# Performance work log

Measured on AMD Instinct MI355X. Metric: run time of the kernel, lower is better.

Reference implementation:

```python
import jax, jax.numpy as jnp
import numpy as np

B, N, M, C, H = 2, 256, 512, 256, 8
Dh = C // H          # head dim = 32
F = 256              # frequency_embedding_size
MAX_PERIOD = 10000.0


def setup_inputs() -> dict:
    rng = jax.random.key(0)
    ks = jax.random.split(rng, 12)
    s = 0.02

    def w(k, shape):
        return jax.random.normal(k, shape, jnp.float32) * s

    inp = {
        "query": jax.random.normal(ks[0], (B, N, C), jnp.float32),
        "key": jax.random.normal(ks[1], (B, M, C), jnp.float32),
        "query_pos": jax.random.uniform(ks[2], (B, N, M), jnp.float32),
        # attention projections (torch Linear stores W as (out,in))
        "Wq": w(ks[3], (C, C)), "bq": jnp.zeros((C,), jnp.float32),
        "Wk": w(ks[4], (C, C)),
        "Wv": w(ks[5], (C, C)), "bv": jnp.zeros((C,), jnp.float32),
        "Wo": w(ks[6], (C, C)), "bo": jnp.zeros((C,), jnp.float32),
        # ScalarEmbedder MLP: Linear(F, C) -> SiLU -> Linear(C, C)
        "W1": w(ks[7], (C, F)), "b1": jnp.zeros((C,), jnp.float32),
        "W2": w(ks[8], (C, C)), "b2": jnp.zeros((C,), jnp.float32),
        "freqs": jnp.exp(-np.log(MAX_PERIOD) * jnp.arange(F // 2, dtype=jnp.float32) / (F // 2)),
    }
    return inp


def reference(query, key, query_pos, Wq, bq, Wk, Wv, bv, Wo, bo, W1, b1, W2, b2, freqs):
    scale = Dh ** (-0.5)
    # projections -> (B, H, N/M, Dh)
    q = (query @ Wq.T + bq).reshape(B, N, H, Dh).transpose(0, 2, 1, 3)
    k = (key @ Wk.T).reshape(B, M, H, Dh).transpose(0, 2, 1, 3)
    v = (key @ Wv.T + bv).reshape(B, M, H, Dh).transpose(0, 2, 1, 3)
    # scalar positional embedding per (n, m) pair
    t = query_pos.reshape(-1)                              # (B*N*M,)
    tf = t[:, None] * freqs                                # (B*N*M, F/2)
    emb = jnp.concatenate([jnp.cos(tf), jnp.sin(tf)], -1)  # (B*N*M, F)
    pe = jax.nn.silu(emb @ W1.T + b1) @ W2.T + b2          # (B*N*M, C)
    pe = pe.reshape(B, N, M, H, Dh).transpose(0, 3, 1, 2, 4)  # (B,H,N,M,Dh)
    # gated scores: (q[:,:,:,None] * pe) . k  ==  einsum over d
    attn = jnp.einsum('bhnd,bhnmd,bhmd->bhnm', q, pe, k) * scale
    attn = jax.nn.softmax(attn, axis=-1)
    x = jnp.einsum('bhnm,bhmd->bhnd', attn, v)             # (B,H,N,Dh)
    x = x.transpose(0, 2, 1, 3).reshape(B, N, C)
    return x @ Wo.T + bo + query
```

## Files before the change

kernel.cpp:

```cpp
#include <hip/hip_runtime.h>

#define Bn 2
#define Nn 256
#define Mn 512
#define Cn 256
#define Hn 8
#define MT 64
#define SCALE_ 0.17677669529663687f

typedef short bf16x8 __attribute__((ext_vector_type(8)));
typedef float f32x4 __attribute__((ext_vector_type(4)));

static __device__ __forceinline__ float b2f(short s) {
    unsigned u = ((unsigned)(unsigned short)s) << 16;
    return __builtin_bit_cast(float, u);
}
static __device__ __forceinline__ short f2b(float f) {
    unsigned u = __builtin_bit_cast(unsigned, f);
    u += 0x7fffu + ((u >> 16) & 1u);
    return (short)(u >> 16);
}
static __device__ __forceinline__ void async16(const void* g, void* l) {
    __builtin_amdgcn_global_load_lds(
        (const __attribute__((address_space(1))) unsigned int*)g,
        (__attribute__((address_space(3))) unsigned int*)l, 16, 0, 0);
}

__global__ void convert_w(const float* __restrict__ W1, const float* __restrict__ W2,
                          short* __restrict__ W1b, short* __restrict__ W2b) {
    int i = blockIdx.x * 256 + threadIdx.x;
    W1b[i] = f2b(W1[i]);
    W2b[i] = f2b(W2[i]);
}

template <bool BF16OUT>
__global__ __launch_bounds__(256) void linear_rc(
        const float* __restrict__ A, const float* __restrict__ W,
        const float* __restrict__ bias, const float* __restrict__ res,
        float* __restrict__ outf, short* __restrict__ outb) {
    __shared__ float arow[32][Cn];
    const int r0 = blockIdx.x * 32;
    const int c0 = blockIdx.y * 64;
    const int t = threadIdx.x;
    #pragma unroll
    for (int i = 0; i < 32; ++i) arow[i][t] = A[(size_t)(r0 + i) * Cn + t];
    __syncthreads();
    const int col = c0 + (t & 63);
    const int rg = (t >> 6) * 8;
    float acc[8];
    #pragma unroll
    for (int i = 0; i < 8; ++i) acc[i] = 0.f;
    const float* wr = W + (size_t)col * Cn;
    for (int k = 0; k < Cn; k += 4) {
        const float4 wv = *(const float4*)(wr + k);
        #pragma unroll
        for (int i = 0; i < 8; ++i)
            acc[i] += arow[rg + i][k] * wv.x + arow[rg + i][k+1] * wv.y
                    + arow[rg + i][k+2] * wv.z + arow[rg + i][k+3] * wv.w;
    }
    const float bv = bias ? bias[col] : 0.f;
    #pragma unroll
    for (int i = 0; i < 8; ++i) {
        float o = acc[i] + bv;
        if (res) o += res[(size_t)(r0 + rg + i) * Cn + col];
        if (BF16OUT) outb[(size_t)(r0 + rg + i) * Cn + col] = f2b(o);
        else         outf[(size_t)(r0 + rg + i) * Cn + col] = o;
    }
}

__global__ __launch_bounds__(256) void linear_kv(
        const float* __restrict__ key, const float* __restrict__ Wk,
        const float* __restrict__ Wv, const float* __restrict__ bv,
        short* __restrict__ kpb, short* __restrict__ vpb) {
    __shared__ float arow[32][Cn];
    const int z = blockIdx.z;
    const float* W = z ? Wv : Wk;
    const float* bias = z ? bv : nullptr;
    short* outb = z ? vpb : kpb;
    const int r0 = blockIdx.x * 32;
    const int c0 = blockIdx.y * 64;
    const int t = threadIdx.x;
    #pragma unroll
    for (int i = 0; i < 32; ++i) arow[i][t] = key[(size_t)(r0 + i) * Cn + t];
    __syncthreads();
    const int col = c0 + (t & 63);
    const int rg = (t >> 6) * 8;
    float acc[8];
    #pragma unroll
    for (int i = 0; i < 8; ++i) acc[i] = 0.f;
    const float* wr = W + (size_t)col * Cn;
    for (int k = 0; k < Cn; k += 4) {
        const float4 wv = *(const float4*)(wr + k);
        #pragma unroll
        for (int i = 0; i < 8; ++i)
            acc[i] += arow[rg + i][k] * wv.x + arow[rg + i][k+1] * wv.y
                    + arow[rg + i][k+2] * wv.z + arow[rg + i][k+3] * wv.w;
    }
    const float bvv = bias ? bias[col] : 0.f;
    #pragma unroll
    for (int i = 0; i < 8; ++i)
        outb[(size_t)(r0 + rg + i) * Cn + col] = f2b(acc[i] + bvv);
}

__global__ __launch_bounds__(512, 1) void fused_attn(
        const float* __restrict__ qp, const short* __restrict__ kpb,
        const short* __restrict__ vpb, const float* __restrict__ qpos,
        const short* __restrict__ W1b, const short* __restrict__ W2b,
        const float* __restrict__ b1, const float* __restrict__ b2,
        const float* __restrict__ freqs, float* __restrict__ xout) {
    __shared__ __align__(16) char embS[MT * 512];
    __shared__ __align__(16) char kS[MT * 512];
    __shared__ __align__(16) char vS[MT * 512];
    __shared__ float tposS[Mn];
    __shared__ float scb2[Hn * MT];
    __shared__ float pacc[512];
    __shared__ float corrS[Hn], lS[Hn];

    const int t = threadIdx.x;
    const int lane = t & 63;
    const int w = t >> 6;
    const int lr = lane & 15, lg = lane >> 4;

    const int qrow = ((blockIdx.x & 7) << 6) | (blockIdx.x >> 3);
    const int b = qrow >> 8;

    bf16x8 w1r[16], w2r[16];
    #pragma unroll
    for (int jb = 0; jb < 2; ++jb) {
        const short* p1 = W1b + (size_t)(w * 32 + jb * 16 + lr) * Cn + lg * 8;
        const short* p2 = W2b + (size_t)(w * 32 + jb * 16 + lr) * Cn + lg * 8;
        #pragma unroll
        for (int kk = 0; kk < 8; ++kk) {
            w1r[jb * 8 + kk] = *(const bf16x8*)(p1 + kk * 32);
            w2r[jb * 8 + kk] = *(const bf16x8*)(p2 + kk * 32);
        }
    }
    const int cA = w * 32 + lr, cB = cA + 16;
    const float b1v0 = b1[cA], b1v1 = b1[cB];
    const float b2v0 = b2[cA], b2v1 = b2[cB];
    const float q0 = qp[(size_t)qrow * Cn + cA];
    const float q1 = qp[(size_t)qrow * Cn + cB];
    const float fv = freqs[t & 127];
    tposS[t] = qpos[(size_t)qrow * Mn + t];
    float m_run = -1e30f, l_run = 0.f;
    float xacc = 0.f;
    const f32x4 vzero = {0.f, 0.f, 0.f, 0.f};
    __syncthreads();

    for (int m0 = 0; m0 < Mn; m0 += MT) {
        {
            const size_t tbase = ((size_t)(b * Mn + m0)) * 512;
            #pragma unroll
            for (int i = 0; i < 4; ++i) {
                const int seg = (i * 8 + w) * 1024;
                async16((const char*)kpb + tbase + seg + lane * 16, kS + seg);
                async16((const char*)vpb + tbase + seg + lane * 16, vS + seg);
            }
        }

        {
            const int f = t & 127, mb = t >> 7;
            #pragma unroll 2
            for (int it = 0; it < 16; ++it) {
                const int m = it * 4 + mb;
                const float tv = tposS[m0 + m];
                float sv, cv;
                __sincosf(tv * fv, &sv, &cv);
                char* rowp = embS + m * 512;
                const int sw = (m & 7) << 4;
                *(short*)(rowp + ((f * 2) ^ sw)) = f2b(cv);
                *(short*)(rowp + ((256 + f * 2) ^ sw)) = f2b(sv);
            }
        }
        __syncthreads();

        f32x4 acc[4][2];
        #pragma unroll
        for (int pb = 0; pb < 4; ++pb) { acc[pb][0] = vzero; acc[pb][1] = vzero; }
        #pragma unroll
        for (int pb = 0; pb < 4; ++pb) {
            const int row = pb * 16 + lr;
            const int sw = (row & 7) << 4;
            const char* rowp = embS + row * 512;
            #pragma unroll
            for (int kk = 0; kk < 8; ++kk) {
                const bf16x8 a = *(const bf16x8*)(rowp + ((lg * 16 + kk * 64) ^ sw));
                acc[pb][0] = __builtin_amdgcn_mfma_f32_16x16x32_bf16(a, w1r[kk],     acc[pb][0], 0, 0, 0);
                acc[pb][1] = __builtin_amdgcn_mfma_f32_16x16x32_bf16(a, w1r[8 + kk], acc[pb][1], 0, 0, 0);
            }
        }
        __syncthreads();

        #pragma unroll
        for (int pb = 0; pb < 4; ++pb) {
            #pragma unroll
            for (int jb = 0; jb < 2; ++jb) {
                const float bv = jb ? b1v1 : b1v0;
                const int j = w * 32 + jb * 16 + lr;
                #pragma unroll
                for (int r = 0; r < 4; ++r) {
                    const int row = pb * 16 + lg * 4 + r;
                    float hv = acc[pb][jb][r] + bv;
                    hv = hv / (1.f + __expf(-hv));
                    *(short*)(embS + row * 512 + ((j * 2) ^ ((row & 7) << 4))) = f2b(hv);
                }
            }
        }
        __syncthreads();

        #pragma unroll
        for (int pb = 0; pb < 4; ++pb) { acc[pb][0] = vzero; acc[pb][1] = vzero; }
        #pragma unroll
        for (int pb = 0; pb < 4; ++pb) {
            const int row = pb * 16 + lr;
            const int sw = (row & 7) << 4;
            const char* rowp = embS + row * 512;
            #pragma unroll
            for (int kk = 0; kk < 8; ++kk) {
                const bf16x8 a = *(const bf16x8*)(rowp + ((lg * 16 + kk * 64) ^ sw));
                acc[pb][0] = __builtin_amdgcn_mfma_f32_16x16x32_bf16(a, w2r[kk],     acc[pb][0], 0, 0, 0);
                acc[pb][1] = __builtin_amdgcn_mfma_f32_16x16x32_bf16(a, w2r[8 + kk], acc[pb][1], 0, 0, 0);
            }
        }

        #pragma unroll
        for (int pb = 0; pb < 4; ++pb) {
            #pragma unroll
            for (int r = 0; r < 4; ++r) {
                const int m = pb * 16 + lg * 4 + r;
                const float k0 = b2f(*(const short*)(kS + m * 512 + cA * 2));
                const float k1 = b2f(*(const short*)(kS + m * 512 + cB * 2));
                float v = (acc[pb][0][r] + b2v0) * q0 * k0
                        + (acc[pb][1][r] + b2v1) * q1 * k1;
                v += __shfl_xor(v, 1);
                v += __shfl_xor(v, 2);
                v += __shfl_xor(v, 4);
                v += __shfl_xor(v, 8);
                if (lr == 0) scb2[w * MT + m] = v * SCALE_;
            }
        }

        {
            const float s = scb2[w * MT + lane];
            float tmax = s;
            #pragma unroll
            for (int msk = 1; msk < 64; msk <<= 1) tmax = fmaxf(tmax, __shfl_xor(tmax, msk));
            const float mnew = fmaxf(m_run, tmax);
            const float corr = __expf(m_run - mnew);
            const float e = __expf(s - mnew);
            scb2[w * MT + lane] = e;
            float ss = e;
            #pragma unroll
            for (int msk = 1; msk < 64; msk <<= 1) ss += __shfl_xor(ss, msk);
            l_run = l_run * corr + ss;
            m_run = mnew;
            if (lane == 0) corrS[w] = corr;
        }
        __syncthreads();

        {
            const int c = t & 255, half = t >> 8;
            const int h = c >> 5;
            const char* vb = vS + (half * 32) * 512 + c * 2;
            const float* wr2 = scb2 + h * MT + half * 32;
            float s = 0.f;
            #pragma unroll 8
            for (int m = 0; m < 32; ++m)
                s += wr2[m] * b2f(*(const short*)(vb + m * 512));
            pacc[t] = s;
        }
        __syncthreads();
        if (t < 256) xacc = xacc * corrS[t >> 5] + pacc[t] + pacc[t + 256];
        __syncthreads();
    }

    if (lane == 0) lS[w] = l_run;
    __syncthreads();
    if (t < 256) xout[(size_t)qrow * Cn + t] = xacc / lS[t >> 5];
}

extern "C" void kernel_launch(void* const* d_in, const int* in_sizes, int n_in,
                              void* d_out, int out_size, void* d_ws, size_t ws_size,
                              hipStream_t stream) {
    const float* query = (const float*)d_in[0];
    const float* key   = (const float*)d_in[1];
    const float* qpos  = (const float*)d_in[2];
    const float* Wq    = (const float*)d_in[3];
    const float* bq    = (const float*)d_in[4];
    const float* Wk    = (const float*)d_in[5];
    const float* Wv    = (const float*)d_in[6];
    const float* bv    = (const float*)d_in[7];
    const float* Wo    = (const float*)d_in[8];
    const float* bo    = (const float*)d_in[9];
    const float* W1    = (const float*)d_in[10];
    const float* b1    = (const float*)d_in[11];
    const float* W2    = (const float*)d_in[12];
    const float* b2    = (const float*)d_in[13];
    const float* freqs = (const float*)d_in[14];
    float* out = (float*)d_out;

    char* ws = (char*)d_ws;
    float* qp  = (float*)(ws);
    short* kpb = (short*)(ws + 524288);
    short* vpb = (short*)(ws + 1048576);
    float* xo  = (float*)(ws + 1572864);
    short* W1b = (short*)(ws + 2097152);
    short* W2b = (short*)(ws + 2228224);

    convert_w<<<256, 256, 0, stream>>>(W1, W2, W1b, W2b);
    linear_rc<false><<<dim3(16, 4), 256, 0, stream>>>(query, Wq, bq, nullptr, qp, nullptr);
    linear_kv<<<dim3(32, 4, 2), 256, 0, stream>>>(key, Wk, Wv, bv, kpb, vpb);
    fused_attn<<<Bn * Nn, 512, 0, stream>>>(qp, kpb, vpb, qpos, W1b, W2b, b1, b2, freqs, xo);
    linear_rc<false><<<dim3(16, 4), 256, 0, stream>>>(xo, Wo, bo, query, out, nullptr);
}
```

Before: 316.4 us.

## Merge prep kernels, transpose K/V layout, vectorize sincos and V reduction

Combines the weight conversion and the Q/K/V projection kernels into one prep launch, and writes K and V transposed (channel-major, bf16) so the attention kernel can do vector LDS reads through a swizzled padded layout. Each thread now computes 16 sincos values for one row and stores them as 16-byte vectors. It also sets waves_per_eu to 2 and pins the weight registers with empty asm. One barrier at the end of the m-loop is dropped. The intent is to cut launch overhead and the scalar LDS traffic in the embedding, score and PV stages. The cost is more registers per thread, and removing the barrier may create a race on pacc and scb2 between iterations.

New measurement: 299.8 us. 1.06x faster.

```diff
diff --git a/kernel.cpp b/kernel.cpp
--- a/kernel.cpp
+++ b/kernel.cpp
@@ -9,6 +9,7 @@
 #define SCALE_ 0.17677669529663687f
 
 typedef short bf16x8 __attribute__((ext_vector_type(8)));
+typedef short bf16x4 __attribute__((ext_vector_type(4)));
 typedef float f32x4 __attribute__((ext_vector_type(4)));
 
 static __device__ __forceinline__ float b2f(short s) {
@@ -25,23 +26,35 @@
         (const __attribute__((address_space(1))) unsigned int*)g,
         (__attribute__((address_space(3))) unsigned int*)l, 16, 0, 0);
 }
-
-__global__ void convert_w(const float* __restrict__ W1, const float* __restrict__ W2,
-                          short* __restrict__ W1b, short* __restrict__ W2b) {
-    int i = blockIdx.x * 256 + threadIdx.x;
-    W1b[i] = f2b(W1[i]);
-    W2b[i] = f2b(W2[i]);
-}
-
-template <bool BF16OUT>
-__global__ __launch_bounds__(256) void linear_rc(
-        const float* __restrict__ A, const float* __restrict__ W,
-        const float* __restrict__ bias, const float* __restrict__ res,
-        float* __restrict__ outf, short* __restrict__ outb) {
+static __device__ __forceinline__ int taddr(int c, int mm) {
+    return (c >> 3) * 1040 + (c & 7) * 128 + (((mm >> 3) ^ (c & 7)) << 4) + (mm & 7) * 2;
+}
+
+__global__ __launch_bounds__(256) void prep(
+        const float* __restrict__ query, const float* __restrict__ key,
+        const float* __restrict__ Wq, const float* __restrict__ bq,
+        const float* __restrict__ Wk, const float* __restrict__ Wv,
+        const float* __restrict__ bv, const float* __restrict__ W1,
+        const float* __restrict__ W2, short* __restrict__ W1b,
+        short* __restrict__ W2b, float* __restrict__ qp,
+        short* __restrict__ kTb, short* __restrict__ vTb) {
     __shared__ float arow[32][Cn];
-    const int r0 = blockIdx.x * 32;
-    const int c0 = blockIdx.y * 64;
+    const int bid = blockIdx.x;
     const int t = threadIdx.x;
+    if (bid < 256) {
+        const int i = bid * 256 + t;
+        W1b[i] = f2b(W1[i]);
+        W2b[i] = f2b(W2[i]);
+        return;
+    }
+    int task, id;
+    if (bid < 320)      { task = 0; id = bid - 256; }
+    else if (bid < 448) { task = 1; id = bid - 320; }
+    else                { task = 2; id = bid - 448; }
+    const int r0 = (id >> 2) * 32;
+    const int c0 = (id & 3) * 64;
+    const float* A = (task == 0) ? query : key;
+    const float* W = (task == 0) ? Wq : (task == 1 ? Wk : Wv);
     #pragma unroll
     for (int i = 0; i < 32; ++i) arow[i][t] = A[(size_t)(r0 + i) * Cn + t];
     __syncthreads();
@@ -58,59 +71,33 @@
             acc[i] += arow[rg + i][k] * wv.x + arow[rg + i][k+1] * wv.y
                     + arow[rg + i][k+2] * wv.z + arow[rg + i][k+3] * wv.w;
     }
-    const float bv = bias ? bias[col] : 0.f;
-    #pragma unroll
-    for (int i = 0; i < 8; ++i) {
-        float o = acc[i] + bv;
-        if (res) o += res[(size_t)(r0 + rg + i) * Cn + col];
-        if (BF16OUT) outb[(size_t)(r0 + rg + i) * Cn + col] = f2b(o);
-        else         outf[(size_t)(r0 + rg + i) * Cn + col] = o;
-    }
-}
-
-__global__ __launch_bounds__(256) void linear_kv(
-        const float* __restrict__ key, const float* __restrict__ Wk,
-        const float* __restrict__ Wv, const float* __restrict__ bv,
-        short* __restrict__ kpb, short* __restrict__ vpb) {
-    __shared__ float arow[32][Cn];
-    const int z = blockIdx.z;
-    const float* W = z ? Wv : Wk;
-    const float* bias = z ? bv : nullptr;
-    short* outb = z ? vpb : kpb;
-    const int r0 = blockIdx.x * 32;
-    const int c0 = blockIdx.y * 64;
-    const int t = threadIdx.x;
-    #pragma unroll
-    for (int i = 0; i < 32; ++i) arow[i][t] = key[(size_t)(r0 + i) * Cn + t];
-    __syncthreads();
-    const int col = c0 + (t & 63);
-    const int rg = (t >> 6) * 8;
-    float acc[8];
-    #pragma unroll
-    for (int i = 0; i < 8; ++i) acc[i] = 0.f;
-    const float* wr = W + (size_t)col * Cn;
-    for (int k = 0; k < Cn; k += 4) {
-        const float4 wv = *(const float4*)(wr + k);
+    if (task == 0) {
+        const float bvv = bq[col];
         #pragma unroll
         for (int i = 0; i < 8; ++i)
-            acc[i] += arow[rg + i][k] * wv.x + arow[rg + i][k+1] * wv.y
-                    + arow[rg + i][k+2] * wv.z + arow[rg + i][k+3] * wv.w;
-    }
-    const float bvv = bias ? bias[col] : 0.f;
-    #pragma unroll
-    for (int i = 0; i < 8; ++i)
-        outb[(size_t)(r0 + rg + i) * Cn + col] = f2b(acc[i] + bvv);
-}
-
-__global__ __launch_bounds__(512, 1) void fused_attn(
-        const float* __restrict__ qp, const short* __restrict__ kpb,
-        const short* __restrict__ vpb, const float* __restrict__ qpos,
+            qp[(size_t)(r0 + rg + i) * Cn + col] = acc[i] + bvv;
+    } else {
+        const float bvv = (task == 2) ? bv[col] : 0.f;
+        short* outb = (task == 2) ? vTb : kTb;
+        const int b = r0 >> 9, mloc = (r0 & 511) + rg;
+        bf16x8 p;
+        #pragma unroll
+        for (int i = 0; i < 8; ++i) p[i] = f2b(acc[i] + bvv);
+        *(bf16x8*)(outb + ((size_t)(b * Cn + col)) * Mn + mloc) = p;
+    }
+}
+
+__global__ __launch_bounds__(512)
+__attribute__((amdgpu_waves_per_eu(2, 2)))
+void fused_attn(
+        const float* __restrict__ qp, const short* __restrict__ kTb,
+        const short* __restrict__ vTb, const float* __restrict__ qpos,
         const short* __restrict__ W1b, const short* __restrict__ W2b,
         const float* __restrict__ b1, const float* __restrict__ b2,
         const float* __restrict__ freqs, float* __restrict__ xout) {
     __shared__ __align__(16) char embS[MT * 512];
-    __shared__ __align__(16) char kS[MT * 512];
-    __shared__ __align__(16) char vS[MT * 512];
+    __shared__ __align__(16) char kTs[32 * 1040];
+    __shared__ __align__(16) char vTs[32 * 1040];
     __shared__ float tposS[Mn];
     __shared__ float scb2[Hn * MT];
     __shared__ float pacc[512];
@@ -135,42 +122,58 @@
             w2r[jb * 8 + kk] = *(const bf16x8*)(p2 + kk * 32);
         }
     }
+    #pragma unroll
+    for (int i = 0; i < 16; ++i) {
+        asm volatile("" : "+v"(w1r[i]));
+        asm volatile("" : "+v"(w2r[i]));
+    }
+
     const int cA = w * 32 + lr, cB = cA + 16;
     const float b1v0 = b1[cA], b1v1 = b1[cB];
     const float b2v0 = b2[cA], b2v1 = b2[cB];
     const float q0 = qp[(size_t)qrow * Cn + cA];
     const float q1 = qp[(size_t)qrow * Cn + cB];
-    const float fv = freqs[t & 127];
+    const int fg = t & 7;
+    float fr[16];
+    #pragma unroll
+    for (int j = 0; j < 16; ++j) fr[j] = freqs[fg * 16 + j];
     tposS[t] = qpos[(size_t)qrow * Mn + t];
     float m_run = -1e30f, l_run = 0.f;
     float xacc = 0.f;
     const f32x4 vzero = {0.f, 0.f, 0.f, 0.f};
+    const int st_c = lane >> 3;
+    const int st_ch = (lane & 7) ^ st_c;
     __syncthreads();
 
     for (int m0 = 0; m0 < Mn; m0 += MT) {
         {
-            const size_t tbase = ((size_t)(b * Mn + m0)) * 512;
+            const size_t gb = (size_t)b * Cn * Mn + m0 + st_ch * 8;
             #pragma unroll
             for (int i = 0; i < 4; ++i) {
-                const int seg = (i * 8 + w) * 1024;
-                async16((const char*)kpb + tbase + seg + lane * 16, kS + seg);
-                async16((const char*)vpb + tbase + seg + lane * 16, vS + seg);
+                const int seg = i * 8 + w;
+                const size_t srow = gb + (size_t)(seg * 8 + st_c) * Mn;
+                async16(kTb + srow, kTs + seg * 1040);
+                async16(vTb + srow, vTs + seg * 1040);
             }
         }
 
         {
-            const int f = t & 127, mb = t >> 7;
-            #pragma unroll 2
-            for (int it = 0; it < 16; ++it) {
-                const int m = it * 4 + mb;
-                const float tv = tposS[m0 + m];
+            const int m = t >> 3;
+            const float tv = tposS[m0 + m];
+            bf16x8 pc[2], ps[2];
+            #pragma unroll
+            for (int j = 0; j < 16; ++j) {
                 float sv, cv;
-                __sincosf(tv * fv, &sv, &cv);
-                char* rowp = embS + m * 512;
-                const int sw = (m & 7) << 4;
-                *(short*)(rowp + ((f * 2) ^ sw)) = f2b(cv);
-                *(short*)(rowp + ((256 + f * 2) ^ sw)) = f2b(sv);
-            }
+                __sincosf(tv * fr[j], &sv, &cv);
+                pc[j >> 3][j & 7] = f2b(cv);
+                ps[j >> 3][j & 7] = f2b(sv);
+            }
+            char* rowp = embS + m * 512;
+            const int sw = (m & 7) << 4;
+            *(bf16x8*)(rowp + ((fg * 32) ^ sw)) = pc[0];
+            *(bf16x8*)(rowp + ((fg * 32 + 16) ^ sw)) = pc[1];
+            *(bf16x8*)(rowp + ((256 + fg * 32) ^ sw)) = ps[0];
+            *(bf16x8*)(rowp + ((256 + fg * 32 + 16) ^ sw)) = ps[1];
         }
         __syncthreads();
 
@@ -225,18 +228,18 @@
 
         #pragma unroll
         for (int pb = 0; pb < 4; ++pb) {
+            const int mmb = pb * 16 + lg * 4;
+            const bf16x4 k4a = *(const bf16x4*)(kTs + taddr(cA, mmb));
+            const bf16x4 k4b = *(const bf16x4*)(kTs + taddr(cB, mmb));
             #pragma unroll
             for (int r = 0; r < 4; ++r) {
-                const int m = pb * 16 + lg * 4 + r;
-                const float k0 = b2f(*(const short*)(kS + m * 512 + cA * 2));
-                const float k1 = b2f(*(const short*)(kS + m * 512 + cB * 2));
-                float v = (acc[pb][0][r] + b2v0) * q0 * k0
-                        + (acc[pb][1][r] + b2v1) * q1 * k1;
+                float v = (acc[pb][0][r] + b2v0) * q0 * b2f(k4a[r])
+                        + (acc[pb][1][r] + b2v1) * q1 * b2f(k4b[r]);
                 v += __shfl_xor(v, 1);
                 v += __shfl_xor(v, 2);
                 v += __shfl_xor(v, 4);
                 v += __shfl_xor(v, 8);
-                if (lr == 0) scb2[w * MT + m] = v * SCALE_;
+                if (lr == 0) scb2[w * MT + mmb + r] = v * SCALE_;
             }
         }
 
@@ -261,22 +264,58 @@
         {
             const int c = t & 255, half = t >> 8;
             const int h = c >> 5;
-            const char* vb = vS + (half * 32) * 512 + c * 2;
+            const int rowb = (c >> 3) * 1040 + (c & 7) * 128;
+            const int c7 = c & 7;
             const float* wr2 = scb2 + h * MT + half * 32;
             float s = 0.f;
-            #pragma unroll 8
-            for (int m = 0; m < 32; ++m)
-                s += wr2[m] * b2f(*(const short*)(vb + m * 512));
+            #pragma unroll
+            for (int i = 0; i < 4; ++i) {
+                const bf16x8 v8 = *(const bf16x8*)(vTs + rowb + (((half * 4 + i) ^ c7) << 4));
+                const float4 wa = *(const float4*)(wr2 + i * 8);
+                const float4 wb = *(const float4*)(wr2 + i * 8 + 4);
+                s += wa.x * b2f(v8[0]) + wa.y * b2f(v8[1]) + wa.z * b2f(v8[2]) + wa.w * b2f(v8[3])
+                   + wb.x * b2f(v8[4]) + wb.y * b2f(v8[5]) + wb.z * b2f(v8[6]) + wb.w * b2f(v8[7]);
+            }
             pacc[t] = s;
         }
         __syncthreads();
         if (t < 256) xacc = xacc * corrS[t >> 5] + pacc[t] + pacc[t + 256];
-        __syncthreads();
     }
 
     if (lane == 0) lS[w] = l_run;
     __syncthreads();
     if (t < 256) xout[(size_t)qrow * Cn + t] = xacc / lS[t >> 5];
+}
+
+__global__ __launch_bounds__(256) void linear_out(
+        const float* __restrict__ A, const float* __restrict__ W,
+        const float* __restrict__ bias, const float* __restrict__ res,
+        float* __restrict__ out) {
+    __shared__ float arow[32][Cn];
+    const int r0 = blockIdx.x * 32;
+    const int c0 = blockIdx.y * 64;
+    const int t = threadIdx.x;
+    #pragma unroll
+    for (int i = 0; i < 32; ++i) arow[i][t] = A[(size_t)(r0 + i) * Cn + t];
+    __syncthreads();
+    const int col = c0 + (t & 63);
+    const int rg = (t >> 6) * 8;
+    float acc[8];
+    #pragma unroll
+    for (int i = 0; i < 8; ++i) acc[i] = 0.f;
+    const float* wr = W + (size_t)col * Cn;
+    for (int k = 0; k < Cn; k += 4) {
+        const float4 wv = *(const float4*)(wr + k);
+        #pragma unroll
+        for (int i = 0; i < 8; ++i)
+            acc[i] += arow[rg + i][k] * wv.x + arow[rg + i][k+1] * wv.y
+                    + arow[rg + i][k+2] * wv.z + arow[rg + i][k+3] * wv.w;
+    }
+    const float bvv = bias[col];
+    #pragma unroll
+    for (int i = 0; i < 8; ++i)
+        out[(size_t)(r0 + rg + i) * Cn + col] =
+            acc[i] + bvv + res[(size_t)(r0 + rg + i) * Cn + col];
 }
 
 extern "C" void kernel_launch(void* const* d_in, const int* in_sizes, int n_in,
@@ -301,15 +340,14 @@
 
     char* ws = (char*)d_ws;
     float* qp  = (float*)(ws);
-    short* kpb = (short*)(ws + 524288);
-    short* vpb = (short*)(ws + 1048576);
+    short* kTb = (short*)(ws + 524288);
+    short* vTb = (short*)(ws + 1048576);
     float* xo  = (float*)(ws + 1572864);
     short* W1b = (short*)(ws + 2097152);
     short* W2b = (short*)(ws + 2228224);
 
-    convert_w<<<256, 256, 0, stream>>>(W1, W2, W1b, W2b);
-    linear_rc<false><<<dim3(16, 4), 256, 0, stream>>>(query, Wq, bq, nullptr, qp, nullptr);
-    linear_kv<<<dim3(32, 4, 2), 256, 0, stream>>>(key, Wk, Wv, bv, kpb, vpb);
-    fused_attn<<<Bn * Nn, 512, 0, stream>>>(qp, kpb, vpb, qpos, W1b, W2b, b1, b2, freqs, xo);
-    linear_rc<false><<<dim3(16, 4), 256, 0, stream>>>(xo, Wo, bo, query, out, nullptr);
-}
+    prep<<<576, 256, 0, stream>>>(query, key, Wq, bq, Wk, Wv, bv, W1, W2,
+                                  W1b, W2b, qp, kTb, vTb);
+    fused_attn<<<Bn * Nn, 512, 0, stream>>>(qp, kTb, vTb, qpos, W1b, W2b, b1, b2, freqs, xo);
+    linear_out<<<dim3(16, 4), 256, 0, stream>>>(xo, Wo, bo, query, out);
+}
```
